# Performance work log

Hardware: AMD Instinct MI355X
Metric: run time of the kernel (lower is better)

## Reference

```python
import jax, jax.numpy as jnp
import numpy as np

B, D, H, W = 4, 40, 40, 40
NPB = 12000            # active voxels per batch item
C0, C1 = 32, 64        # nPlanes = [32, 64]
BLOCK_REPS = 2
EPS = 1e-4             # BatchNorm eps used by the gorilla-3d norm_fn


def _subm_pairs(coords, dims):
    # indice pairs for 3x3x3 submanifold conv: for kernel offset k,
    # out[j] += f[i] @ W[k] where coord_j = coord_i + offset_k and both voxels are active
    D_, H_, W_ = dims
    b, z, y, x = coords[:, 0], coords[:, 1], coords[:, 2], coords[:, 3]
    lin = ((b * D_ + z) * H_ + y) * W_ + x  # sorted unique linear ids
    ins, outs = [], []
    for dz in (-1, 0, 1):
        for dy in (-1, 0, 1):
            for dx in (-1, 0, 1):
                nz, ny, nx = z + dz, y + dy, x + dx
                valid = (nz >= 0) & (nz < D_) & (ny >= 0) & (ny < H_) & (nx >= 0) & (nx < W_)
                tgt = ((b * D_ + nz) * H_ + ny) * W_ + nx
                pos = np.clip(np.searchsorted(lin, tgt), 0, len(lin) - 1)
                found = valid & (lin[pos] == tgt)
                ins.append(np.nonzero(found)[0].astype(np.int32))
                outs.append(pos[found].astype(np.int32))
    return ins, outs


def _down_pairs(coords, dims):
    # indice pairs for 2x2x2 stride-2 SparseConv3d; output voxels = unique(coord // 2)
    D_, H_, W_ = dims
    D2, H2, W2 = (D_ + 1) // 2, (H_ + 1) // 2, (W_ + 1) // 2
    b, z, y, x = coords[:, 0], coords[:, 1], coords[:, 2], coords[:, 3]
    plin = ((b * D2 + z // 2) * H2 + y // 2) * W2 + x // 2
    ulin, inv = np.unique(plin, return_inverse=True)
    k = (z % 2) * 4 + (y % 2) * 2 + (x % 2)  # which of the 8 kernel taps
    ins = [np.nonzero(k == kk)[0].astype(np.int32) for kk in range(8)]
    outs = [inv[m].astype(np.int32) for m in ins]
    t = ulin.copy()
    x1 = t % W2; t //= W2; y1 = t % H2; t //= H2; z1 = t % D2; b1 = t // D2
    coords1 = np.stack([b1, z1, y1, x1], 1).astype(np.int64)
    return ins, outs, coords1, (D2, H2, W2)


def _pad_pairs(ins, outs, pad_in, pad_out):
    K = len(ins); P = max(max(len(p) for p in ins), 1)
    A = np.full((K, P), pad_in, np.int32)
    O = np.full((K, P), pad_out, np.int32)
    for kk in range(K):
        A[kk, :len(ins[kk])] = ins[kk]
        O[kk, :len(outs[kk])] = outs[kk]
    return jnp.asarray(A), jnp.asarray(O)


def setup_inputs():
    rng = np.random.default_rng(0)
    coords = []
    for b in range(B):
        lin = np.sort(rng.choice(D * H * W, NPB, replace=False))
        z = lin // (H * W); y = (lin // W) % H; x = lin % W
        coords.append(np.stack([np.full(NPB, b), z, y, x], 1))
    coords = np.concatenate(coords).astype(np.int64)
    n0 = coords.shape[0]
    s0i, s0o = _subm_pairs(coords, (D, H, W))
    subm0_in, subm0_out = _pad_pairs(s0i, s0o, n0, n0)
    di, do, coords1, dims1 = _down_pairs(coords, (D, H, W))
    n1 = int(coords1.shape[0])
    down_in, down_out = _pad_pairs(di, do, n0, n1)
    s1i, s1o = _subm_pairs(coords1, dims1)
    subm1_in, subm1_out = _pad_pairs(s1i, s1o, n1, n1)

    keys = iter(jax.random.split(jax.random.key(0), 128))

    def bn_p(c):
        g = 1.0 + 0.1 * jax.random.normal(next(keys), (c,))
        be = 0.1 * jax.random.normal(next(keys), (c,))
        m = 0.1 * jax.random.normal(next(keys), (c,))
        v = jax.random.uniform(next(keys), (c,), minval=0.5, maxval=1.5)
        return jnp.stack([g, be, m, v]).astype(jnp.float32)

    def w(shape):
        fan = shape[-2] * (shape[-3] if len(shape) >= 3 else 1)
        return (jax.random.normal(next(keys), shape) / np.sqrt(fan)).astype(jnp.float32)

    return dict(
        feats=jax.random.normal(next(keys), (n0, C0), dtype=jnp.float32),
        res0_W=w((BLOCK_REPS, 2, 27, C0, C0)),
        res0_bn=jnp.stack([jnp.stack([bn_p(C0), bn_p(C0)]) for _ in range(BLOCK_REPS)]),
        down_bn=bn_p(C0), down_W=w((8, C0, C1)),
        res1_W=w((BLOCK_REPS, 2, 27, C1, C1)),
        res1_bn=jnp.stack([jnp.stack([bn_p(C1), bn_p(C1)]) for _ in range(BLOCK_REPS)]),
        up_bn=bn_p(C1), up_W=w((8, C1, C0)),
        tail0_bn1=bn_p(2 * C0), tail0_W1=w((27, 2 * C0, C0)),
        tail0_bn2=bn_p(C0), tail0_W2=w((27, C0, C0)),
        tail0_Wsc=w((2 * C0, C0)),
        tail1_W=w((2, 27, C0, C0)),
        tail1_bn=jnp.stack([bn_p(C0), bn_p(C0)]),
        subm0_in=subm0_in, subm0_out=subm0_out,
        subm1_in=subm1_in, subm1_out=subm1_out,
        down_in=down_in, down_out=down_out,
        n1=n1,
    )


def _bn_relu(x, p):
    # BatchNorm1d (eval mode, running stats) followed by ReLU; p is [4, C] = (gamma, beta, mean, var)
    g, b, m, v = p
    return jax.nn.relu((x - m) * (g * jax.lax.rsqrt(v + EPS)) + b)


def _sparse_conv(x, Wk, pin, pout, n_out):
    # gather-matmul-scatter over padded indice pairs.
    # x: [Nin, Cin], Wk: [K, Cin, Cout], pin/pout: [K, P] (padded with sentinel Nin / n_out)
    x_ext = jnp.concatenate([x, jnp.zeros((1, x.shape[1]), x.dtype)], 0)
    g = x_ext[pin]                                   # [K, P, Cin]
    c = jnp.einsum('kpc,kcd->kpd', g, Wk)            # [K, P, Cout]
    out = jnp.zeros((n_out + 1, Wk.shape[2]), x.dtype)
    out = out.at[pout.reshape(-1)].add(c.reshape(-1, Wk.shape[2]))
    return out[:n_out]


def _res_block(x, Ws, bns, pin, pout, n, Wsc=None):
    # ResidualBlock: (norm, relu, subm3x3, norm, relu, subm3x3) + identity/1x1 shortcut
    idt = x if Wsc is None else x @ Wsc
    h = _bn_relu(x, bns[0]); h = _sparse_conv(h, Ws[0], pin, pout, n)
    h = _bn_relu(h, bns[1]); h = _sparse_conv(h, Ws[1], pin, pout, n)
    return h + idt


def _forward(feats, res0_W, res0_bn, down_bn, down_W, res1_W, res1_bn, up_bn, up_W,
             tail0_bn1, tail0_W1, tail0_bn2, tail0_W2, tail0_Wsc, tail1_W, tail1_bn,
             subm0_in, subm0_out, subm1_in, subm1_out, down_in, down_out, n1):
    n0 = feats.shape[0]
    x = feats
    for i in range(BLOCK_REPS):                       # self.blocks
        x = _res_block(x, res0_W[i], res0_bn[i], subm0_in, subm0_out, n0)
    identity = x                                      # identity SparseConvTensor
    # self.conv: norm, relu, SparseConv3d(k=2, s=2)
    x1 = _sparse_conv(_bn_relu(x, down_bn), down_W, down_in, down_out, n1)
    for i in range(BLOCK_REPS):                       # self.u (leaf UBlock) blocks
        x1 = _res_block(x1, res1_W[i], res1_bn[i], subm1_in, subm1_out, n1)
    # self.deconv: norm, relu, SparseInverseConv3d (same pairs, roles swapped)
    dec = _sparse_conv(_bn_relu(x1, up_bn), up_W, down_out, down_in, n0)
    x = jnp.concatenate([identity, dec], 1)           # [N0, 2*C0]
    # blocks_tail: block0 (2*C0 -> C0, 1x1 shortcut), block1 (C0 -> C0)
    h = _bn_relu(x, tail0_bn1); h = _sparse_conv(h, tail0_W1, subm0_in, subm0_out, n0)
    h = _bn_relu(h, tail0_bn2); h = _sparse_conv(h, tail0_W2, subm0_in, subm0_out, n0)
    x = h + x @ tail0_Wsc
    x = _res_block(x, tail1_W, tail1_bn, subm0_in, subm0_out, n0)
    return x


def reference(feats, res0_W, res0_bn, down_bn, down_W, res1_W, res1_bn, up_bn, up_W,
              tail0_bn1, tail0_W1, tail0_bn2, tail0_W2, tail0_Wsc, tail1_W, tail1_bn,
              subm0_in, subm0_out, subm1_in, subm1_out, down_in, down_out, n1):
    return _forward(feats, res0_W, res0_bn, down_bn, down_W, res1_W, res1_bn, up_bn, up_W,
                    tail0_bn1, tail0_W1, tail0_bn2, tail0_W2, tail0_Wsc, tail1_W, tail1_bn,
                    subm0_in, subm0_out, subm1_in, subm1_out, down_in, down_out, n1)
```

## Files before the change

kernel.cpp:

```cpp
#include <hip/hip_runtime.h>

#define EPS_BN 1e-4f

typedef _Float16 f16x8 __attribute__((ext_vector_type(8)));
typedef float f32x4 __attribute__((ext_vector_type(4)));

template <int C>
__global__ __launch_bounds__(256) void bn_relu_kernel(
    const float* __restrict__ x, const float* __restrict__ bn,
    _Float16* __restrict__ out, int n_const, const int* __restrict__ n_dev)
{
    const int n = n_dev ? *n_dev : n_const;
    const long total = (long)n * C;
    const long i = (long)blockIdx.x * blockDim.x + threadIdx.x;
    if (i >= total) return;
    const int c = (int)(i & (C - 1));
    const float g = bn[c], b = bn[C + c], m = bn[2 * C + c], v = bn[3 * C + c];
    const float val = (x[i] - m) * (g * rsqrtf(v + EPS_BN)) + b;
    out[i] = (_Float16)fmaxf(val, 0.f);
}

__global__ __launch_bounds__(256) void build_table_kernel(
    const int* __restrict__ pin, const int* __restrict__ pout,
    int K, int P, int pad_const, const int* __restrict__ pad_dev,
    int KPAD, int* __restrict__ T)
{
    const int e = blockIdx.x * 256 + threadIdx.x;
    if (e >= K * P) return;
    const int pad = pad_dev ? *pad_dev : pad_const;
    const int in = pin[e];
    if (in == pad) return;
    const int k = e / P;
    T[(size_t)pout[e] * KPAD + k] = in;
}

struct WSeg { const float* src; _Float16* dst; int tot, ci, co; };
struct WAll { WSeg s[7]; };

__global__ __launch_bounds__(256) void wcvt_all_kernel(WAll w)
{
    const WSeg sg = w.s[blockIdx.y];
    const int per = sg.ci * sg.co;
    for (int e = blockIdx.x * 256 + threadIdx.x; e < sg.tot; e += gridDim.x * 256) {
        const int k = e / per, r = e % per;
        const int ci = r / sg.co, co = r % sg.co;
        sg.dst[(size_t)k * per + (size_t)co * sg.ci + ci] = (_Float16)sg.src[e];
    }
}

template <int CIN, int COUT, int K, int KPAD, int WR, int WC, int M_REP,
          int TG, int MINW>
__global__ __launch_bounds__(256, MINW) void mconv_kernel(
    const _Float16* __restrict__ x, const _Float16* __restrict__ Wt,
    const int* __restrict__ Trow,
    const float* __restrict__ add, float* __restrict__ fout,
    const float* __restrict__ bnx, _Float16* __restrict__ hout,
    int n_const, const int* __restrict__ n_dev)
{
    static_assert(K % TG == 0, "K must be divisible by TG");
    static_assert(WR * WC == 4, "4 waves");
    constexpr int BM = WR * M_REP * 16;
    constexpr int KK = CIN / 32;
    constexpr int SEGS = CIN / 8;
    constexpr int SLOTS = BM * SEGS;
    constexpr int SPT = (SLOTS + 255) / 256;
    constexpr int NP = K / TG;
    __shared__ _Float16 A[2][TG * SLOTS * 8];
    __shared__ int TL[BM * K];

    const int n = n_dev ? *n_dev : n_const;
    const int row0 = blockIdx.x * BM;
    if (row0 >= n) return;

    const int tid = threadIdx.x;
    const int wave = tid >> 6, lane = tid & 63;
    const int lrow = lane & 15, g = lane >> 4;
    const int wr = wave / WC, wc = wave % WC;

    for (int idx = tid; idx < BM * K; idx += 256) {
        const int r = idx / K, k = idx % K;
        TL[idx] = (row0 + r < n) ? Trow[(size_t)(row0 + r) * KPAD + k] : -1;
    }
    __syncthreads();

    auto stage_issue = [&](int p, f16x8 (&v)[TG][SPT]) {
#pragma unroll
        for (int s = 0; s < SPT; ++s) {
            const int f = tid + s * 256;
            if (f < SLOTS) {
                const int q = f >> 6;
                const int kk = q % KK;
                const int r = (q / KK) * 16 + (f & 15);
                const int seg = kk * 4 + ((f >> 4) & 3);
#pragma unroll
                for (int tg = 0; tg < TG; ++tg) {
                    const int t = TL[r * K + (p * TG + tg)];
                    v[tg][s] = (t >= 0)
                        ? *(const f16x8*)(x + (size_t)t * CIN + seg * 8)
                        : (f16x8)(_Float16)0.f;
                }
            }
        }
    };
    auto stage_write = [&](int buf, f16x8 (&v)[TG][SPT]) {
#pragma unroll
        for (int s = 0; s < SPT; ++s) {
            const int f = tid + s * 256;
            if (f < SLOTS) {
#pragma unroll
                for (int tg = 0; tg < TG; ++tg)
                    *(f16x8*)(&A[buf][(tg * SLOTS + f) * 8]) = v[tg][s];
            }
        }
    };

    f32x4 acc[M_REP];
#pragma unroll
    for (int m = 0; m < M_REP; ++m) acc[m] = (f32x4)0.f;

    {
        f16x8 st[TG][SPT];
        stage_issue(0, st);
        stage_write(0, st);
    }
    __syncthreads();

    for (int p = 0; p < NP; ++p) {
        f16x8 nst[TG][SPT];
        if (p + 1 < NP) stage_issue(p + 1, nst);

        const _Float16* Ab = A[p & 1];
        __builtin_amdgcn_s_setprio(1);
#pragma unroll
        for (int tg = 0; tg < TG; ++tg) {
            const int tap = p * TG + tg;
            const _Float16* wb = Wt + ((size_t)tap * COUT + wc * 16 + lrow) * CIN
                               + g * 8;
            f16x8 b[KK];
#pragma unroll
            for (int kk = 0; kk < KK; ++kk)
                b[kk] = *(const f16x8*)(wb + kk * 32);
#pragma unroll
            for (int m = 0; m < M_REP; ++m)
#pragma unroll
                for (int kk = 0; kk < KK; ++kk) {
                    const int a16 = tg * SLOTS + ((wr * M_REP + m) * KK + kk) * 64
                                  + lane;
                    const f16x8 av = *(const f16x8*)(&Ab[a16 * 8]);
                    acc[m] = __builtin_amdgcn_mfma_f32_16x16x32_f16(
                        av, b[kk], acc[m], 0, 0, 0);
                }
        }
        __builtin_amdgcn_s_setprio(0);

        if (p + 1 < NP) stage_write((p + 1) & 1, nst);
        __syncthreads();
    }

#pragma unroll
    for (int m = 0; m < M_REP; ++m) {
        const int rbase = row0 + (wr * M_REP + m) * 16 + g * 4;
        const int c = wc * 16 + lrow;
        float sc = 0.f, mm = 0.f, be = 0.f;
        if (hout) {
            const float ga = bnx[c], va = bnx[3 * COUT + c];
            be = bnx[COUT + c];
            mm = bnx[2 * COUT + c];
            sc = ga * rsqrtf(va + EPS_BN);
        }
#pragma unroll
        for (int i = 0; i < 4; ++i) {
            const int r = rbase + i;
            if (r < n) {
                const size_t o = (size_t)r * COUT + c;
                float v = acc[m][i];
                if (add) v += add[o];
                if (fout) fout[o] = v;
                if (hout) hout[o] = (_Float16)fmaxf((v - mm) * sc + be, 0.f);
            }
        }
    }
}

__global__ __launch_bounds__(256) void concat_bn_kernel(
    const float* __restrict__ a, const float* __restrict__ b,
    float* __restrict__ fout, const float* __restrict__ bnx,
    _Float16* __restrict__ hout, int n)
{
    const int i = blockIdx.x * 256 + threadIdx.x;
    if (i >= n * 64) return;
    const int row = i >> 6, c = i & 63;
    const float v = (c < 32) ? a[row * 32 + c] : b[row * 32 + (c - 32)];
    fout[i] = v;
    const float g = bnx[c], be = bnx[64 + c], m = bnx[128 + c], va = bnx[192 + c];
    hout[i] = (_Float16)fmaxf((v - m) * (g * rsqrtf(va + EPS_BN)) + be, 0.f);
}

__global__ __launch_bounds__(256) void dense_mm_kernel(
    const float* __restrict__ x, const float* __restrict__ W,
    float* __restrict__ out, int n)
{
    __shared__ float Wl[64 * 32];
    for (int i = threadIdx.x; i < 64 * 32; i += 256) Wl[i] = W[i];
    __syncthreads();
    const int idx = blockIdx.x * 256 + threadIdx.x;
    const int row = idx >> 5, c = idx & 31;
    if (row >= n) return;
    const float* xr = x + (size_t)row * 64;
    float acc = 0.f;
#pragma unroll
    for (int q = 0; q < 16; ++q) {
        const float4 xv = *(const float4*)(xr + 4 * q);
        acc = fmaf(xv.x, Wl[(4 * q + 0) * 32 + c], acc);
        acc = fmaf(xv.y, Wl[(4 * q + 1) * 32 + c], acc);
        acc = fmaf(xv.z, Wl[(4 * q + 2) * 32 + c], acc);
        acc = fmaf(xv.w, Wl[(4 * q + 3) * 32 + c], acc);
    }
    out[(size_t)row * 32 + c] = acc;
}


extern "C" void kernel_launch(void* const* d_in, const int* in_sizes, int n_in,
                              void* d_out, int out_size, void* d_ws, size_t ws_size,
                              hipStream_t stream)
{
    const float* feats   = (const float*)d_in[0];
    const float* res0_W  = (const float*)d_in[1];
    const float* res0_bn = (const float*)d_in[2];
    const float* down_bn = (const float*)d_in[3];
    const float* down_W  = (const float*)d_in[4];
    const float* res1_W  = (const float*)d_in[5];
    const float* res1_bn = (const float*)d_in[6];
    const float* up_bn   = (const float*)d_in[7];
    const float* up_W    = (const float*)d_in[8];
    const float* t0_bn1  = (const float*)d_in[9];
    const float* t0_W1   = (const float*)d_in[10];
    const float* t0_bn2  = (const float*)d_in[11];
    const float* t0_W2   = (const float*)d_in[12];
    const float* t0_Wsc  = (const float*)d_in[13];
    const float* t1_W    = (const float*)d_in[14];
    const float* t1_bn   = (const float*)d_in[15];
    const int* s0i = (const int*)d_in[16];
    const int* s0o = (const int*)d_in[17];
    const int* s1i = (const int*)d_in[18];
    const int* s1o = (const int*)d_in[19];
    const int* dni = (const int*)d_in[20];
    const int* dno = (const int*)d_in[21];
    const int* n1p = (const int*)d_in[22];

    const int n0 = in_sizes[0] / 32;
    const int P0 = in_sizes[16] / 27;
    const int P1 = in_sizes[18] / 27;
    const int Pd = in_sizes[20] / 8;

    const size_t bufN = (size_t)n0 * 64;
    float* F1 = (float*)d_ws;
    float* F2 = F1 + bufN;
    float* F3 = F2 + bufN;
    float* F4 = F3 + bufN;
    _Float16* Ha = (_Float16*)(F4 + bufN);
    _Float16* Hb = Ha + bufN;
    int* T0r = (int*)(Hb + bufN);
    int* T1r = T0r + (size_t)n0 * 28;
    int* Tdr = T1r + (size_t)n0 * 28;
    int* Tur = Tdr + (size_t)n0 * 8;
    _Float16* Wt_res0 = (_Float16*)(Tur + (size_t)n0 * 8);
    _Float16* Wt_down = Wt_res0 + 108 * 1024;
    _Float16* Wt_res1 = Wt_down + 8 * 2048;
    _Float16* Wt_up   = Wt_res1 + (size_t)108 * 4096;
    _Float16* Wt_t01  = Wt_up + 8 * 2048;
    _Float16* Wt_t02  = Wt_t01 + 27 * 2048;
    _Float16* Wt_t1   = Wt_t02 + 27 * 1024;

    hipMemsetAsync(T0r, 0xFF, (size_t)n0 * 72 * 4, stream);
    auto build = [&](const int* pin, const int* pout, int K, int P,
                     int padc, const int* padd, int KPAD, int* T) {
        hipLaunchKernelGGL(build_table_kernel, dim3((K * P + 255) / 256),
                           dim3(256), 0, stream, pin, pout, K, P, padc, padd,
                           KPAD, T);
    };
    build(s0i, s0o, 27, P0, n0, nullptr, 28, T0r);
    build(s1i, s1o, 27, P1, 0, n1p, 28, T1r);
    build(dni, dno, 8, Pd, n0, nullptr, 8, Tdr);
    build(dno, dni, 8, Pd, 0, n1p, 8, Tur);

    WAll wa;
    wa.s[0] = {res0_W, Wt_res0, 108 * 1024, 32, 32};
    wa.s[1] = {down_W, Wt_down, 8 * 2048, 32, 64};
    wa.s[2] = {res1_W, Wt_res1, 108 * 4096, 64, 64};
    wa.s[3] = {up_W,   Wt_up,   8 * 2048, 64, 32};
    wa.s[4] = {t0_W1,  Wt_t01,  27 * 2048, 64, 32};
    wa.s[5] = {t0_W2,  Wt_t02,  27 * 1024, 32, 32};
    wa.s[6] = {t1_W,   Wt_t1,   54 * 1024, 32, 32};
    hipLaunchKernelGGL(wcvt_all_kernel, dim3((108 * 4096 + 255) / 256, 7),
                       dim3(256), 0, stream, wa);

    const int g32 = (n0 * 32 + 255) / 256;
    const int g64 = (n0 * 64 + 255) / 256;
    const int gm64 = (n0 + 63) / 64;
    const int gm32 = (n0 + 31) / 32;

    auto mc3232 = [&](const _Float16* xin, const _Float16* Wtp, const int* T,
                      const float* add, float* fo, const float* bn, _Float16* ho,
                      int nc, const int* nd) {
        hipLaunchKernelGGL((mconv_kernel<32, 32, 27, 28, 2, 2, 2, 3, 4>),
                           dim3(gm64), dim3(256), 0, stream,
                           xin, Wtp, T, add, fo, bn, ho, nc, nd);
    };
    auto mc6464 = [&](const _Float16* xin, const _Float16* Wtp,
                      const float* add, float* fo, const float* bn, _Float16* ho) {
        hipLaunchKernelGGL((mconv_kernel<64, 64, 27, 28, 1, 4, 2, 3, 4>),
                           dim3(gm32), dim3(256), 0, stream,
                           xin, Wtp, T1r, add, fo, bn, ho, 0, n1p);
    };

    hipLaunchKernelGGL((bn_relu_kernel<32>), dim3(g32), dim3(256), 0, stream,
                       feats, res0_bn + 0 * 128, Ha, n0, nullptr);
    mc3232(Ha, Wt_res0 + 0 * 27 * 1024, T0r, nullptr, nullptr,
           res0_bn + 1 * 128, Hb, n0, nullptr);
    mc3232(Hb, Wt_res0 + 1 * 27 * 1024, T0r, feats, F2,
           res0_bn + 2 * 128, Ha, n0, nullptr);
    mc3232(Ha, Wt_res0 + 2 * 27 * 1024, T0r, nullptr, nullptr,
           res0_bn + 3 * 128, Hb, n0, nullptr);
    mc3232(Hb, Wt_res0 + 3 * 27 * 1024, T0r, F2, F3, down_bn, Ha, n0, nullptr);
    hipLaunchKernelGGL((mconv_kernel<32, 64, 8, 8, 1, 4, 2, 2, 4>),
                       dim3(gm32), dim3(256), 0, stream, Ha, Wt_down, Tdr,
                       (const float*)nullptr, F1, res1_bn + 0 * 256, Hb, 0, n1p);
    mc6464(Hb, Wt_res1 + 0 * 27 * 4096, nullptr, nullptr, res1_bn + 1 * 256, Ha);
    mc6464(Ha, Wt_res1 + 1 * 27 * 4096, F1, F4, res1_bn + 2 * 256, Hb);
    mc6464(Hb, Wt_res1 + 2 * 27 * 4096, nullptr, nullptr, res1_bn + 3 * 256, Ha);
    mc6464(Ha, Wt_res1 + 3 * 27 * 4096, F4, F1, up_bn, Hb);
    hipLaunchKernelGGL((mconv_kernel<64, 32, 8, 8, 2, 2, 1, 2, 4>),
                       dim3(gm32), dim3(256), 0, stream, Hb, Wt_up, Tur,
                       (const float*)nullptr, F2, (const float*)nullptr,
                       (_Float16*)nullptr, n0, nullptr);
    hipLaunchKernelGGL(concat_bn_kernel, dim3(g64), dim3(256), 0, stream,
                       F3, F2, F4, t0_bn1, Ha, n0);
    hipLaunchKernelGGL((mconv_kernel<64, 32, 27, 28, 2, 2, 1, 3, 4>),
                       dim3(gm32), dim3(256), 0, stream, Ha, Wt_t01, T0r,
                       (const float*)nullptr, (float*)nullptr, t0_bn2, Hb,
                       n0, nullptr);
    hipLaunchKernelGGL(dense_mm_kernel, dim3(g32), dim3(256), 0, stream,
                       F4, t0_Wsc, F2, n0);
    mc3232(Hb, Wt_t02, T0r, F2, F2, t1_bn + 0 * 128, Ha, n0, nullptr);
    mc3232(Ha, Wt_t1 + 0 * 27 * 1024, T0r, nullptr, nullptr,
           t1_bn + 1 * 128, Hb, n0, nullptr);
    mc3232(Hb, Wt_t1 + 1 * 27 * 1024, T0r, F2, (float*)d_out,
           nullptr, nullptr, n0, nullptr);
}
```

Before: 511.0 us.

## Deepen gather prefetch to two phases and prefetch weight fragments in registers

Restructures the sparse-conv MFMA main loop so that gathered input rows are issued two phases ahead, using two register staging sets, and weight fragments for the next phase are loaded into registers while the current one computes. The end-of-phase __syncthreads is replaced with an explicit lgkmcnt wait plus s_barrier wrapped in sched_barriers, and the phase loop is fully unrolled. The aim is to hide global gather and weight-load latency behind MFMA work. The cost is much higher register pressure from two A staging sets and a B set, which may reduce occupancy or cause spills.

```diff
diff --git a/kernel.cpp b/kernel.cpp
--- a/kernel.cpp
+++ b/kernel.cpp
@@ -59,6 +59,7 @@
 {
     static_assert(K % TG == 0, "K must be divisible by TG");
     static_assert(WR * WC == 4, "4 waves");
+    static_assert(WC * 16 == COUT, "wave covers one 16-cout slice");
     constexpr int BM = WR * M_REP * 16;
     constexpr int KK = CIN / 32;
     constexpr int SEGS = CIN / 8;
@@ -113,33 +114,45 @@
             }
         }
     };
-
-    f32x4 acc[M_REP];
-#pragma unroll
-    for (int m = 0; m < M_REP; ++m) acc[m] = (f32x4)0.f;
-
-    {
-        f16x8 st[TG][SPT];
-        stage_issue(0, st);
-        stage_write(0, st);
-    }
-    __syncthreads();
-
-    for (int p = 0; p < NP; ++p) {
-        f16x8 nst[TG][SPT];
-        if (p + 1 < NP) stage_issue(p + 1, nst);
-
-        const _Float16* Ab = A[p & 1];
-        __builtin_amdgcn_s_setprio(1);
+    auto bload = [&](int p, f16x8 (&b)[TG][KK]) {
 #pragma unroll
         for (int tg = 0; tg < TG; ++tg) {
             const int tap = p * TG + tg;
             const _Float16* wb = Wt + ((size_t)tap * COUT + wc * 16 + lrow) * CIN
                                + g * 8;
-            f16x8 b[KK];
 #pragma unroll
             for (int kk = 0; kk < KK; ++kk)
-                b[kk] = *(const f16x8*)(wb + kk * 32);
+                b[tg][kk] = *(const f16x8*)(wb + kk * 32);
+        }
+    };
+
+    f32x4 acc[M_REP];
+#pragma unroll
+    for (int m = 0; m < M_REP; ++m) acc[m] = (f32x4)0.f;
+
+    f16x8 sA0[TG][SPT], sA1[TG][SPT];
+    f16x8 sB[TG][KK];
+
+    stage_issue(0, sA0);
+    if (NP > 1) stage_issue(1, sA1);
+    bload(0, sB);
+    stage_write(0, sA0);
+    asm volatile("s_waitcnt lgkmcnt(0)" ::: "memory");
+    __builtin_amdgcn_sched_barrier(0);
+    __builtin_amdgcn_s_barrier();
+    __builtin_amdgcn_sched_barrier(0);
+
+#pragma unroll
+    for (int p = 0; p < NP; ++p) {
+        if (p + 2 < NP) {
+            if (p & 1) stage_issue(p + 2, sA1);
+            else       stage_issue(p + 2, sA0);
+        }
+
+        const _Float16* Ab = A[p & 1];
+        __builtin_amdgcn_s_setprio(1);
+#pragma unroll
+        for (int tg = 0; tg < TG; ++tg)
 #pragma unroll
             for (int m = 0; m < M_REP; ++m)
 #pragma unroll
@@ -148,13 +161,20 @@
                                   + lane;
                     const f16x8 av = *(const f16x8*)(&Ab[a16 * 8]);
                     acc[m] = __builtin_amdgcn_mfma_f32_16x16x32_f16(
-                        av, b[kk], acc[m], 0, 0, 0);
+                        av, sB[tg][kk], acc[m], 0, 0, 0);
                 }
-        }
         __builtin_amdgcn_s_setprio(0);
 
-        if (p + 1 < NP) stage_write((p + 1) & 1, nst);
-        __syncthreads();
+        if (p + 1 < NP) bload(p + 1, sB);
+
+        if (p + 1 < NP) {
+            if (p & 1) stage_write((p + 1) & 1, sA0);
+            else       stage_write((p + 1) & 1, sA1);
+            asm volatile("s_waitcnt lgkmcnt(0)" ::: "memory");
+            __builtin_amdgcn_sched_barrier(0);
+            __builtin_amdgcn_s_barrier();
+            __builtin_amdgcn_sched_barrier(0);
+        }
     }
 
 #pragma unroll
```

Result: no change. 518.3 us (+1.4%).

## Stage per-tap weights in swizzled LDS and pipeline one tap per iteration

Applied to the files above, without the earlier changes.

The sparse conv kernel now processes one kernel tap per loop iteration instead of groups of TG taps. The weight tile for the next tap is double-buffered in LDS with an XOR swizzle, where before each wave read it directly from global memory. The smaller A buffer frees LDS, and the occupancy hint (MINW) rises from 4 to 8 for several launches. The cost is more iterations and barriers per block, plus extra LDS traffic for the weights.

```diff
diff --git a/kernel.cpp b/kernel.cpp
--- a/kernel.cpp
+++ b/kernel.cpp
@@ -49,7 +49,7 @@
 }
 
 template <int CIN, int COUT, int K, int KPAD, int WR, int WC, int M_REP,
-          int TG, int MINW>
+          int MINW>
 __global__ __launch_bounds__(256, MINW) void mconv_kernel(
     const _Float16* __restrict__ x, const _Float16* __restrict__ Wt,
     const int* __restrict__ Trow,
@@ -57,15 +57,17 @@
     const float* __restrict__ bnx, _Float16* __restrict__ hout,
     int n_const, const int* __restrict__ n_dev)
 {
-    static_assert(K % TG == 0, "K must be divisible by TG");
     static_assert(WR * WC == 4, "4 waves");
+    static_assert(WC * 16 == COUT, "wave covers one 16-cout slice");
     constexpr int BM = WR * M_REP * 16;
     constexpr int KK = CIN / 32;
-    constexpr int SEGS = CIN / 8;
-    constexpr int SLOTS = BM * SEGS;
-    constexpr int SPT = (SLOTS + 255) / 256;
-    constexpr int NP = K / TG;
-    __shared__ _Float16 A[2][TG * SLOTS * 8];
+    constexpr int SLOTS_A = BM * (CIN / 8);
+    constexpr int SLOTS_B = CIN * COUT / 8;
+    constexpr int SPT_B = (SLOTS_B + 255) / 256;
+    constexpr int ROWSLOT = CIN / 8;
+    static_assert(SLOTS_A <= 256, "one A slot per thread");
+    __shared__ _Float16 Abuf[2][SLOTS_A * 8];
+    __shared__ _Float16 Bbuf[2][SLOTS_B * 8];
     __shared__ int TL[BM * K];
 
     const int n = n_dev ? *n_dev : n_const;
@@ -83,77 +85,79 @@
     }
     __syncthreads();
 
-    auto stage_issue = [&](int p, f16x8 (&v)[TG][SPT]) {
-#pragma unroll
-        for (int s = 0; s < SPT; ++s) {
-            const int f = tid + s * 256;
-            if (f < SLOTS) {
-                const int q = f >> 6;
-                const int kk = q % KK;
-                const int r = (q / KK) * 16 + (f & 15);
-                const int seg = kk * 4 + ((f >> 4) & 3);
-#pragma unroll
-                for (int tg = 0; tg < TG; ++tg) {
-                    const int t = TL[r * K + (p * TG + tg)];
-                    v[tg][s] = (t >= 0)
-                        ? *(const f16x8*)(x + (size_t)t * CIN + seg * 8)
-                        : (f16x8)(_Float16)0.f;
-                }
+    const int qa   = tid >> 6;
+    const int kka  = qa % KK;
+    const int ra   = (qa / KK) * 16 + (tid & 15);
+    const int sega = kka * 4 + ((tid >> 4) & 3);
+
+    auto issueA = [&](int k, f16x8& v) {
+        if (tid < SLOTS_A) {
+            const int t = TL[ra * K + k];
+            v = (t >= 0) ? *(const f16x8*)(x + (size_t)t * CIN + sega * 8)
+                         : (f16x8)(_Float16)0.f;
+        }
+    };
+    auto writeA = [&](int buf, const f16x8& v) {
+        if (tid < SLOTS_A) *(f16x8*)(&Abuf[buf][tid * 8]) = v;
+    };
+    auto issueB = [&](int k, f16x8 (&v)[SPT_B]) {
+        const _Float16* wt = Wt + (size_t)k * CIN * COUT;
+#pragma unroll
+        for (int s = 0; s < SPT_B; ++s) {
+            const int fb = tid + s * 256;
+            if (fb < SLOTS_B) v[s] = *(const f16x8*)(wt + fb * 8);
+        }
+    };
+    auto writeB = [&](int buf, const f16x8 (&v)[SPT_B]) {
+#pragma unroll
+        for (int s = 0; s < SPT_B; ++s) {
+            const int fb = tid + s * 256;
+            if (fb < SLOTS_B) {
+                const int cob = fb / ROWSLOT;
+                const int sw = fb ^ (cob & 7);
+                *(f16x8*)(&Bbuf[buf][sw * 8]) = v[s];
             }
         }
     };
-    auto stage_write = [&](int buf, f16x8 (&v)[TG][SPT]) {
-#pragma unroll
-        for (int s = 0; s < SPT; ++s) {
-            const int f = tid + s * 256;
-            if (f < SLOTS) {
-#pragma unroll
-                for (int tg = 0; tg < TG; ++tg)
-                    *(f16x8*)(&A[buf][(tg * SLOTS + f) * 8]) = v[tg][s];
+
+    f32x4 acc[M_REP];
+#pragma unroll
+    for (int m = 0; m < M_REP; ++m) acc[m] = (f32x4)0.f;
+
+    f16x8 sA;
+    f16x8 sB[SPT_B];
+
+    issueA(0, sA);
+    issueB(0, sB);
+    writeA(0, sA);
+    writeB(0, sB);
+    __syncthreads();
+
+    const int co = wc * 16 + lrow;
+    for (int p = 0; p < K; ++p) {
+        if (p + 1 < K) { issueA(p + 1, sA); issueB(p + 1, sB); }
+
+        const int buf = p & 1;
+        f16x8 bv[KK];
+#pragma unroll
+        for (int kk = 0; kk < KK; ++kk) {
+            const int s = co * ROWSLOT + kk * 4 + g;
+            const int sw = s ^ (co & 7);
+            bv[kk] = *(const f16x8*)(&Bbuf[buf][sw * 8]);
+        }
+        __builtin_amdgcn_s_setprio(1);
+#pragma unroll
+        for (int m = 0; m < M_REP; ++m)
+#pragma unroll
+            for (int kk = 0; kk < KK; ++kk) {
+                const int a16 = ((wr * M_REP + m) * KK + kk) * 64 + lane;
+                const f16x8 av = *(const f16x8*)(&Abuf[buf][a16 * 8]);
+                acc[m] = __builtin_amdgcn_mfma_f32_16x16x32_f16(
+                    av, bv[kk], acc[m], 0, 0, 0);
             }
-        }
-    };
-
-    f32x4 acc[M_REP];
-#pragma unroll
-    for (int m = 0; m < M_REP; ++m) acc[m] = (f32x4)0.f;
-
-    {
-        f16x8 st[TG][SPT];
-        stage_issue(0, st);
-        stage_write(0, st);
-    }
-    __syncthreads();
-
-    for (int p = 0; p < NP; ++p) {
-        f16x8 nst[TG][SPT];
-        if (p + 1 < NP) stage_issue(p + 1, nst);
-
-        const _Float16* Ab = A[p & 1];
-        __builtin_amdgcn_s_setprio(1);
-#pragma unroll
-        for (int tg = 0; tg < TG; ++tg) {
-            const int tap = p * TG + tg;
-            const _Float16* wb = Wt + ((size_t)tap * COUT + wc * 16 + lrow) * CIN
-                               + g * 8;
-            f16x8 b[KK];
-#pragma unroll
-            for (int kk = 0; kk < KK; ++kk)
-                b[kk] = *(const f16x8*)(wb + kk * 32);
-#pragma unroll
-            for (int m = 0; m < M_REP; ++m)
-#pragma unroll
-                for (int kk = 0; kk < KK; ++kk) {
-                    const int a16 = tg * SLOTS + ((wr * M_REP + m) * KK + kk) * 64
-                                  + lane;
-                    const f16x8 av = *(const f16x8*)(&Ab[a16 * 8]);
-                    acc[m] = __builtin_amdgcn_mfma_f32_16x16x32_f16(
-                        av, b[kk], acc[m], 0, 0, 0);
-                }
-        }
         __builtin_amdgcn_s_setprio(0);
 
-        if (p + 1 < NP) stage_write((p + 1) & 1, nst);
+        if (p + 1 < K) { writeA(buf ^ 1, sA); writeB(buf ^ 1, sB); }
         __syncthreads();
     }
 
@@ -303,13 +307,13 @@
     auto mc3232 = [&](const _Float16* xin, const _Float16* Wtp, const int* T,
                       const float* add, float* fo, const float* bn, _Float16* ho,
                       int nc, const int* nd) {
-        hipLaunchKernelGGL((mconv_kernel<32, 32, 27, 28, 2, 2, 2, 3, 4>),
+        hipLaunchKernelGGL((mconv_kernel<32, 32, 27, 28, 2, 2, 2, 8>),
                            dim3(gm64), dim3(256), 0, stream,
                            xin, Wtp, T, add, fo, bn, ho, nc, nd);
     };
     auto mc6464 = [&](const _Float16* xin, const _Float16* Wtp,
                       const float* add, float* fo, const float* bn, _Float16* ho) {
-        hipLaunchKernelGGL((mconv_kernel<64, 64, 27, 28, 1, 4, 2, 3, 4>),
+        hipLaunchKernelGGL((mconv_kernel<64, 64, 27, 28, 1, 4, 2, 4>),
                            dim3(gm32), dim3(256), 0, stream,
                            xin, Wtp, T1r, add, fo, bn, ho, 0, n1p);
     };
@@ -323,20 +327,20 @@
     mc3232(Ha, Wt_res0 + 2 * 27 * 1024, T0r, nullptr, nullptr,
            res0_bn + 3 * 128, Hb, n0, nullptr);
     mc3232(Hb, Wt_res0 + 3 * 27 * 1024, T0r, F2, F3, down_bn, Ha, n0, nullptr);
-    hipLaunchKernelGGL((mconv_kernel<32, 64, 8, 8, 1, 4, 2, 2, 4>),
+    hipLaunchKernelGGL((mconv_kernel<32, 64, 8, 8, 1, 4, 2, 8>),
                        dim3(gm32), dim3(256), 0, stream, Ha, Wt_down, Tdr,
                        (const float*)nullptr, F1, res1_bn + 0 * 256, Hb, 0, n1p);
     mc6464(Hb, Wt_res1 + 0 * 27 * 4096, nullptr, nullptr, res1_bn + 1 * 256, Ha);
     mc6464(Ha, Wt_res1 + 1 * 27 * 4096, F1, F4, res1_bn + 2 * 256, Hb);
     mc6464(Hb, Wt_res1 + 2 * 27 * 4096, nullptr, nullptr, res1_bn + 3 * 256, Ha);
     mc6464(Ha, Wt_res1 + 3 * 27 * 4096, F4, F1, up_bn, Hb);
-    hipLaunchKernelGGL((mconv_kernel<64, 32, 8, 8, 2, 2, 1, 2, 4>),
+    hipLaunchKernelGGL((mconv_kernel<64, 32, 8, 8, 2, 2, 1, 8>),
                        dim3(gm32), dim3(256), 0, stream, Hb, Wt_up, Tur,
                        (const float*)nullptr, F2, (const float*)nullptr,
                        (_Float16*)nullptr, n0, nullptr);
     hipLaunchKernelGGL(concat_bn_kernel, dim3(g64), dim3(256), 0, stream,
                        F3, F2, F4, t0_bn1, Ha, n0);
-    hipLaunchKernelGGL((mconv_kernel<64, 32, 27, 28, 2, 2, 1, 3, 4>),
+    hipLaunchKernelGGL((mconv_kernel<64, 32, 27, 28, 2, 2, 1, 8>),
                        dim3(gm32), dim3(256), 0, stream, Ha, Wt_t01, T0r,
                        (const float*)nullptr, (float*)nullptr, t0_bn2, Hb,
                        n0, nullptr);
```

Result: faster. 471.1 us (-7.8%).
